# Optimization experiments

Measured on AMD Instinct MI355X. Metric: run time of the kernel, lower is better.

The kernel has to match this reference:

```python
import jax, jax.numpy as jnp
import numpy as np

NU, NI, E = 200000, 100000, 500000
D, H, O = 128, 256, 128  # embedding_dim, hidden_dim, output_dim


def _sage(x_src, x_dst, src, dst, n_dst, W_l, b_l, W_r):
    """PyG SAGEConv (mean aggr): lin_l(mean_j x_src[j]) + lin_r(x_dst)."""
    msgs = x_src[src]                                            # [E, d_in]
    summed = jax.ops.segment_sum(msgs, dst, num_segments=n_dst)  # [n_dst, d_in]
    deg = jax.ops.segment_sum(jnp.ones(src.shape, x_src.dtype), dst, num_segments=n_dst)
    mean = summed / jnp.maximum(deg, 1.0)[:, None]
    return mean @ W_l + b_l + x_dst @ W_r


def setup_inputs() -> dict:
    key = jax.random.key(0)
    ks = jax.random.split(key, 18)

    def w(k, i, o):
        return jax.random.normal(k, (i, o), jnp.float32) / np.float32(np.sqrt(i))

    return {
        "x_user": jax.random.normal(ks[0], (NU, D), jnp.float32),
        "x_item": jax.random.normal(ks[1], (NI, D), jnp.float32),
        "edge_src": jax.random.randint(ks[2], (E,), 0, NU, jnp.int32),
        "edge_dst": jax.random.randint(ks[3], (E,), 0, NI, jnp.int32),
        # layer 1 (encoder): D -> H, one SAGEConv per edge type
        "W_l1_ui": w(ks[4], D, H), "W_r1_ui": w(ks[5], D, H), "b_l1_ui": jnp.zeros((H,), jnp.float32),
        "W_l1_iu": w(ks[6], D, H), "W_r1_iu": w(ks[7], D, H), "b_l1_iu": jnp.zeros((H,), jnp.float32),
        # layer 2 (projection): H -> O
        "W_l2_ui": w(ks[8], H, O), "W_r2_ui": w(ks[9], H, O), "b_l2_ui": jnp.zeros((O,), jnp.float32),
        "W_l2_iu": w(ks[10], H, O), "W_r2_iu": w(ks[11], H, O), "b_l2_iu": jnp.zeros((O,), jnp.float32),
    }


def reference(x_user, x_item, edge_src, edge_dst,
              W_l1_ui, W_r1_ui, b_l1_ui, W_l1_iu, W_r1_iu, b_l1_iu,
              W_l2_ui, W_r2_ui, b_l2_ui, W_l2_iu, W_r2_iu, b_l2_iu):
    # encoder layer: relu(SAGEConv) per destination node type (dropout=eval/no-op)
    h_item = jax.nn.relu(_sage(x_user, x_item, edge_src, edge_dst, NI, W_l1_ui, b_l1_ui, W_r1_ui))
    h_user = jax.nn.relu(_sage(x_item, x_user, edge_dst, edge_src, NU, W_l1_iu, b_l1_iu, W_r1_iu))
    # extra relu in RecommendationGNN.forward is a no-op after relu
    # projection layer: relu(SAGEConv), dropout=0
    o_item = jax.nn.relu(_sage(h_user, h_item, edge_src, edge_dst, NI, W_l2_ui, b_l2_ui, W_r2_ui))
    o_user = jax.nn.relu(_sage(h_item, h_user, edge_dst, edge_src, NU, W_l2_iu, b_l2_iu, W_r2_iu))
    return (o_user, o_item)
```

## Files before the change

kernel.cpp:

```cpp
#include <hip/hip_runtime.h>
#include <stdint.h>

typedef __attribute__((ext_vector_type(8))) short short8;
typedef __attribute__((ext_vector_type(4))) float f32x4;

#define SCAN_TILE 4096

__device__ __forceinline__ float bf2f(unsigned short u) {
  union { unsigned int i; float f; } v;
  v.i = ((unsigned int)u) << 16;
  return v.f;
}
__device__ __forceinline__ unsigned short f2bf(float f) {
  union { float f; unsigned int i; } v;
  v.f = f;
  unsigned int u = v.i;
  return (unsigned short)((u + 0x7FFFu + ((u >> 16) & 1u)) >> 16);
}
__device__ __forceinline__ unsigned int pack2(float a, float b) {
  return (unsigned int)f2bf(a) | ((unsigned int)f2bf(b) << 16);
}
__device__ __forceinline__ void add2(float& a, float& b, unsigned int v) {
  a += bf2f((unsigned short)(v & 0xffff));
  b += bf2f((unsigned short)(v >> 16));
}

__device__ __forceinline__ size_t fragS128(int row, int k) {
  return ((size_t)(row >> 4) * 4 + (size_t)(k >> 5)) * 512
       + (size_t)((((row & 15) + (((k >> 3) & 3) << 4)) << 3) + (k & 7));
}

__global__ __launch_bounds__(256) void build_wt_all(
    const float* __restrict__ Wl1ui, const float* __restrict__ Wr1ui,
    const float* __restrict__ Wl1iu, const float* __restrict__ Wr1iu,
    const float* __restrict__ Wl2ui, const float* __restrict__ Wr2ui,
    const float* __restrict__ Wl2iu, const float* __restrict__ Wr2iu,
    unsigned short* __restrict__ T1ui_l, unsigned short* __restrict__ T1ui_h,
    unsigned short* __restrict__ T1iu_l, unsigned short* __restrict__ T1iu_h,
    unsigned short* __restrict__ T2lui_l, unsigned short* __restrict__ T2lui_h,
    unsigned short* __restrict__ T2rui_l, unsigned short* __restrict__ T2rui_h,
    unsigned short* __restrict__ T2liu_l, unsigned short* __restrict__ T2liu_h,
    unsigned short* __restrict__ T2riu_l, unsigned short* __restrict__ T2riu_h)
{
  int idx = blockIdx.x * 256 + threadIdx.x;
  const float *W1, *W2;
  unsigned short *lo, *hi;
  int N, rel;
  if (idx < 65536)       { W1 = Wl1ui; W2 = Wr1ui;          lo = T1ui_l;  hi = T1ui_h;  N = 256; rel = idx; }
  else if (idx < 131072) { W1 = Wl1iu; W2 = Wr1iu;          lo = T1iu_l;  hi = T1iu_h;  N = 256; rel = idx - 65536; }
  else if (idx < 163840) { W1 = Wl2ui; W2 = Wl2ui + 128*128; lo = T2lui_l; hi = T2lui_h; N = 128; rel = idx - 131072; }
  else if (idx < 196608) { W1 = Wr2ui; W2 = Wr2ui + 128*128; lo = T2rui_l; hi = T2rui_h; N = 128; rel = idx - 163840; }
  else if (idx < 229376) { W1 = Wl2iu; W2 = Wl2iu + 128*128; lo = T2liu_l; hi = T2liu_h; N = 128; rel = idx - 196608; }
  else                   { W1 = Wr2iu; W2 = Wr2iu + 128*128; lo = T2riu_l; hi = T2riu_h; N = 128; rel = idx - 229376; }
  int n = rel >> 8;
  int k = rel & 255;
  float v = (k < 128) ? W1[(size_t)k * N + n] : W2[(size_t)(k - 128) * N + n];
  if (k < 128) lo[fragS128(n, k)] = f2bf(v);
  else         hi[fragS128(n, k - 128)] = f2bf(v);
}

__global__ __launch_bounds__(256) void conv_x(
    const float* __restrict__ xu, const float* __restrict__ xi,
    uint4* __restrict__ XfI, uint4* __restrict__ XfU,
    int NI, int NU, int MI, int MU)
{
  int u = blockIdx.x * 256 + threadIdx.x;
  int unitsI = MI * 16;
  const float* x; uint4* Xf; int M; int rel;
  if (u < unitsI) { x = xi; Xf = XfI; M = NI; rel = u; }
  else {
    rel = u - unitsI;
    if (rel >= MU * 16) return;
    x = xu; Xf = XfU; M = NU;
  }
  int c = rel >> 6;
  int s = rel & 63;
  int row = ((c >> 2) << 4) + (s & 15);
  int k = ((c & 3) << 5) + ((s >> 4) << 3);
  uint4 o = make_uint4(0u, 0u, 0u, 0u);
  if (row < M) {
    f32x4 a = *(const f32x4*)(x + (size_t)row * 128 + k);
    f32x4 b = *(const f32x4*)(x + (size_t)row * 128 + k + 4);
    o.x = pack2(a[0], a[1]); o.y = pack2(a[2], a[3]);
    o.z = pack2(b[0], b[1]); o.w = pack2(b[2], b[3]);
  }
  Xf[rel] = o;
}

__global__ __launch_bounds__(256) void hist(
    const int* __restrict__ esrc, const int* __restrict__ edst,
    int* __restrict__ cntAll, int NI, int E)
{
  int e = blockIdx.x * 256 + threadIdx.x;
  if (e >= E) return;
  atomicAdd(&cntAll[edst[e]], 1);
  atomicAdd(&cntAll[NI + esrc[e]], 1);
}

__global__ __launch_bounds__(256) void scan_p1(
    const int* __restrict__ cnt, int* __restrict__ tileSums, int NA)
{
  __shared__ int red[256];
  int b = blockIdx.x, t = threadIdx.x;
  int base = b * SCAN_TILE;
  int s = 0;
  for (int i = t; i < SCAN_TILE; i += 256) {
    int g = base + i;
    if (g < NA) s += cnt[g];
  }
  red[t] = s;
  __syncthreads();
  for (int d = 128; d > 0; d >>= 1) {
    if (t < d) red[t] += red[t + d];
    __syncthreads();
  }
  if (t == 0) tileSums[b] = red[0];
}

__global__ __launch_bounds__(256) void scan_p2(
    int* __restrict__ tileSums, int nTiles, int* __restrict__ offEnd)
{
  __shared__ int buf[256];
  int t = threadIdx.x;
  int v = (t < nTiles) ? tileSums[t] : 0;
  buf[t] = v;
  __syncthreads();
  for (int d = 1; d < 256; d <<= 1) {
    int x = (t >= d) ? buf[t - d] : 0;
    __syncthreads();
    buf[t] += x;
    __syncthreads();
  }
  if (t < nTiles) tileSums[t] = buf[t] - v;
  if (t == nTiles - 1) *offEnd = buf[t];
}

__global__ __launch_bounds__(256) void scan_p3(
    const int* __restrict__ cnt, const int* __restrict__ tileSums,
    int* __restrict__ off, int NA)
{
  __shared__ int red[256];
  int b = blockIdx.x, t = threadIdx.x;
  int base = b * SCAN_TILE + t * 16;
  int loc[16];
  int s = 0;
#pragma unroll
  for (int i = 0; i < 16; ++i) {
    int g = base + i;
    loc[i] = (g < NA) ? cnt[g] : 0;
    s += loc[i];
  }
  red[t] = s;
  __syncthreads();
  for (int d = 1; d < 256; d <<= 1) {
    int x = (t >= d) ? red[t - d] : 0;
    __syncthreads();
    red[t] += x;
    __syncthreads();
  }
  int run = tileSums[b] + red[t] - s;
#pragma unroll
  for (int i = 0; i < 16; ++i) {
    int g = base + i;
    if (g < NA) off[g] = run;
    run += loc[i];
  }
}

__global__ __launch_bounds__(256) void fill_idx(
    const int* __restrict__ esrc, const int* __restrict__ edst,
    const int* __restrict__ offAll, int* __restrict__ curAll,
    int* __restrict__ idxAll, int NI, int E)
{
  int e = blockIdx.x * 256 + threadIdx.x;
  if (e >= E) return;
  int s = esrc[e], d = edst[e];
  int pI = offAll[d] + atomicAdd(&curAll[d], 1);
  idxAll[pI] = s;
  int pU = offAll[NI + s] + atomicAdd(&curAll[NI + s], 1);
  idxAll[pU] = d;
}

__global__ __launch_bounds__(256) void build_mean(
    const float* __restrict__ xu, const float* __restrict__ xi,
    const int* __restrict__ idxAll, const int* __restrict__ offAll,
    unsigned short* __restrict__ MfI, unsigned short* __restrict__ MfU,
    int NI, int NA)
{
  int w2 = (blockIdx.x * 256 + threadIdx.x) >> 6;
  int l = threadIdx.x & 63;
  int h = l >> 5;
  int lh = l & 31;
  int node = w2 * 2 + h;
  if (node >= NA) return;
  bool isItem = (node < NI);
  const float* xo = isItem ? xu : xi;
  unsigned short* Mf = isItem ? MfI : MfU;
  int n = isItem ? node : (node - NI);
  int s = offAll[node], e = offAll[node + 1];

  f32x4 acc = (f32x4){0.f, 0.f, 0.f, 0.f};
  int j = s;
  for (; j + 1 < e; j += 2) {
    int g0 = idxAll[j];
    int g1 = idxAll[j + 1];
    f32x4 v0 = *(const f32x4*)(xo + (size_t)g0 * 128 + lh * 4);
    f32x4 v1 = *(const f32x4*)(xo + (size_t)g1 * 128 + lh * 4);
    acc += v0 + v1;
  }
  if (j < e) {
    int g = idxAll[j];
    acc += *(const f32x4*)(xo + (size_t)g * 128 + lh * 4);
  }

  float inv = 1.0f / (float)max(e - s, 1);
  uint2 o;
  o.x = pack2(acc[0] * inv, acc[1] * inv);
  o.y = pack2(acc[2] * inv, acc[3] * inv);
  *(uint2*)(Mf + fragS128(n, lh * 4)) = o;
}

__global__ __launch_bounds__(256) void seg_mean(
    const unsigned int* __restrict__ pU, const unsigned int* __restrict__ pI,
    const int* __restrict__ idxAll, const int* __restrict__ offAll,
    unsigned int* __restrict__ m2I, unsigned int* __restrict__ m2U,
    int NI, int NA)
{
  int w4 = (blockIdx.x * 256 + threadIdx.x) >> 6;
  int l = threadIdx.x & 63;
  int q = l >> 4;
  int lq = l & 15;
  int node = w4 * 4 + q;
  if (node >= NA) return;
  bool isItem = (node < NI);
  const unsigned int* p = isItem ? pU : pI;
  unsigned int* m2 = isItem ? m2I : m2U;
  int n = isItem ? node : (node - NI);
  int s = offAll[node], e = offAll[node + 1];

  float a0 = 0.f, a1 = 0.f, a2 = 0.f, a3 = 0.f,
        a4 = 0.f, a5 = 0.f, a6 = 0.f, a7 = 0.f;

  int j = s;
  for (; j + 1 < e; j += 2) {
    int g0 = idxAll[j];
    int g1 = idxAll[j + 1];
    uint4 v0 = *(const uint4*)(p + (size_t)g0 * 64 + lq * 4);
    uint4 v1 = *(const uint4*)(p + (size_t)g1 * 64 + lq * 4);
    add2(a0, a1, v0.x); add2(a2, a3, v0.y); add2(a4, a5, v0.z); add2(a6, a7, v0.w);
    add2(a0, a1, v1.x); add2(a2, a3, v1.y); add2(a4, a5, v1.z); add2(a6, a7, v1.w);
  }
  if (j < e) {
    int g = idxAll[j];
    uint4 v = *(const uint4*)(p + (size_t)g * 64 + lq * 4);
    add2(a0, a1, v.x); add2(a2, a3, v.y); add2(a4, a5, v.z); add2(a6, a7, v.w);
  }

  float inv = 1.0f / (float)max(e - s, 1);
  uint4 o;
  o.x = pack2(a0 * inv, a1 * inv);
  o.y = pack2(a2 * inv, a3 * inv);
  o.z = pack2(a4 * inv, a5 * inv);
  o.w = pack2(a6 * inv, a7 * inv);
  *(uint4*)(m2 + (size_t)n * 64 + lq * 4) = o;
}

struct GemmP {
  const unsigned short* Alo; const unsigned short* Ahi;
  const unsigned short* Blo; const unsigned short* Bhi;
  const float* bias;
  const unsigned short* Madd;
  void* outp; unsigned short* outHi;
  int M;
};

__global__ __launch_bounds__(256) void gemm_flat(
    GemmP P0, GemmP P1, int rb0,
    int outF32, int outFrag, int N, int doRelu)
{
  __shared__ __attribute__((aligned(16))) uint4 lds4[2048];

  const int bx = blockIdx.x;
  const bool first = (bx < rb0);
  GemmP P = first ? P0 : P1;
  const int mb = first ? bx : bx - rb0;

  const int tid = threadIdx.x;
  const int lane = tid & 63;
  const int wave = tid >> 6;
  const int nBase = blockIdx.y * 128;
  const int r16 = lane & 15;
  const int quad = lane >> 4;

  const uint4* AL = (const uint4*)P.Alo;
  const uint4* AH = (const uint4*)P.Ahi;
  const uint4* BL = (const uint4*)P.Blo + (size_t)(nBase >> 4) * 256;
  const uint4* BH = (const uint4*)P.Bhi + (size_t)(nBase >> 4) * 256;

  const int fa = wave * 2;

#define STAGE(s, b) do {                                                        \
    const uint4* As_ = ((s) < 4 ? AL : AH);                                     \
    const uint4* Bs_ = ((s) < 4 ? BL : BH);                                     \
    const int k0_ = (s) & 3;                                                    \
    const uint4* ga0 = As_ + ((size_t)((mb * 8 + fa) * 4 + k0_)) * 64 + lane;   \
    const uint4* ga1 = As_ + ((size_t)((mb * 8 + fa + 1) * 4 + k0_)) * 64 + lane;\
    const uint4* gb0 = Bs_ + ((size_t)(fa * 4 + k0_)) * 64 + lane;              \
    const uint4* gb1 = Bs_ + ((size_t)((fa + 1) * 4 + k0_)) * 64 + lane;        \
    __builtin_amdgcn_global_load_lds(                                           \
        (const __attribute__((address_space(1))) void*)ga0,                     \
        (__attribute__((address_space(3))) void*)&lds4[(b) * 1024 + fa * 64], 16, 0, 0); \
    __builtin_amdgcn_global_load_lds(                                           \
        (const __attribute__((address_space(1))) void*)ga1,                     \
        (__attribute__((address_space(3))) void*)&lds4[(b) * 1024 + (fa + 1) * 64], 16, 0, 0); \
    __builtin_amdgcn_global_load_lds(                                           \
        (const __attribute__((address_space(1))) void*)gb0,                     \
        (__attribute__((address_space(3))) void*)&lds4[(b) * 1024 + 512 + fa * 64], 16, 0, 0); \
    __builtin_amdgcn_global_load_lds(                                           \
        (const __attribute__((address_space(1))) void*)gb1,                     \
        (__attribute__((address_space(3))) void*)&lds4[(b) * 1024 + 512 + (fa + 1) * 64], 16, 0, 0); \
  } while (0)

  f32x4 acc[4][4];
#pragma unroll
  for (int i = 0; i < 4; ++i)
#pragma unroll
    for (int j = 0; j < 4; ++j) acc[i][j] = (f32x4){0.f, 0.f, 0.f, 0.f};

  STAGE(0, 0);
  STAGE(1, 1);

  const int wr = (wave >> 1) * 4;
  const int wc = (wave & 1) * 4;

#pragma unroll
  for (int s = 0; s < 8; ++s) {
    const int b = s & 1;
    if (s < 7) asm volatile("s_waitcnt vmcnt(4)\ns_barrier" ::: "memory");
    else       asm volatile("s_waitcnt vmcnt(0)\ns_barrier" ::: "memory");

    short8 av[4], bv[4];
#pragma unroll
    for (int g = 0; g < 4; ++g) {
      uint4 ta = lds4[b * 1024 + (wr + g) * 64 + lane];
      uint4 tb = lds4[b * 1024 + 512 + (wc + g) * 64 + lane];
      av[g] = *(const short8*)&ta;
      bv[g] = *(const short8*)&tb;
    }
#pragma unroll
    for (int mg = 0; mg < 4; ++mg)
#pragma unroll
      for (int ng = 0; ng < 4; ++ng)
        acc[mg][ng] = __builtin_amdgcn_mfma_f32_16x16x32_bf16(bv[ng], av[mg], acc[mg][ng], 0, 0, 0);

    if (s < 6) {
      asm volatile("s_waitcnt lgkmcnt(0)\ns_barrier" ::: "memory");
      STAGE(s + 2, b);
    }
  }
#undef STAGE

  const int m0 = mb * 128 + (wave >> 1) * 64;
  const int n0 = nBase + (wave & 1) * 64;
#pragma unroll
  for (int mg = 0; mg < 4; ++mg) {
    int row = m0 + mg * 16 + r16;
    if (row < P.M) {
#pragma unroll
      for (int ng = 0; ng < 4; ++ng) {
        int col = n0 + ng * 16 + quad * 4;
        f32x4 v = acc[mg][ng];
        if (P.bias) {
          f32x4 b4 = *(const f32x4*)(P.bias + col);
          v += b4;
        }
        if (P.Madd) {
          uint2 md = *(const uint2*)(P.Madd + (size_t)row * 128 + col);
          v[0] += bf2f((unsigned short)(md.x & 0xffff));
          v[1] += bf2f((unsigned short)(md.x >> 16));
          v[2] += bf2f((unsigned short)(md.y & 0xffff));
          v[3] += bf2f((unsigned short)(md.y >> 16));
        }
        if (doRelu) {
          v[0] = fmaxf(v[0], 0.0f); v[1] = fmaxf(v[1], 0.0f);
          v[2] = fmaxf(v[2], 0.0f); v[3] = fmaxf(v[3], 0.0f);
        }
        if (outF32) {
          *(f32x4*)((float*)P.outp + (size_t)row * N + col) = v;
        } else {
          uint2 o;
          o.x = pack2(v[0], v[1]);
          o.y = pack2(v[2], v[3]);
          if (outFrag) {
            if (col < 128) *(uint2*)((unsigned short*)P.outp + fragS128(row, col)) = o;
            else           *(uint2*)(P.outHi + fragS128(row, col - 128)) = o;
          } else {
            *(uint2*)((unsigned short*)P.outp + (size_t)row * N + col) = o;
          }
        }
      }
    }
  }
}

extern "C" void kernel_launch(void* const* d_in, const int* in_sizes, int n_in,
                              void* d_out, int out_size, void* d_ws, size_t ws_size,
                              hipStream_t stream)
{
  const float* x_user  = (const float*)d_in[0];
  const float* x_item  = (const float*)d_in[1];
  const int*   esrc    = (const int*)d_in[2];
  const int*   edst    = (const int*)d_in[3];
  const float* W_l1_ui = (const float*)d_in[4];
  const float* W_r1_ui = (const float*)d_in[5];
  const float* b_l1_ui = (const float*)d_in[6];
  const float* W_l1_iu = (const float*)d_in[7];
  const float* W_r1_iu = (const float*)d_in[8];
  const float* b_l1_iu = (const float*)d_in[9];
  const float* W_l2_ui = (const float*)d_in[10];
  const float* W_r2_ui = (const float*)d_in[11];
  const float* b_l2_ui = (const float*)d_in[12];
  const float* W_l2_iu = (const float*)d_in[13];
  const float* W_r2_iu = (const float*)d_in[14];
  const float* b_l2_iu = (const float*)d_in[15];

  const int NU = in_sizes[0] / 128;
  const int NI = in_sizes[1] / 128;
  const int E  = in_sizes[2];
  const int NA = NI + NU;
  const int MI = ((NI + 127) / 128) * 128;
  const int MU = ((NU + 127) / 128) * 128;

  char* ws = (char*)d_ws;
  size_t off = 0;
  auto alloc = [&](size_t bytes) -> void* {
    void* p = ws + off;
    off += (bytes + 255) & ~(size_t)255;
    return p;
  };

  int* cntAll = (int*)alloc((size_t)NA * 4);
  int* curAll = (int*)alloc((size_t)NA * 4);
  size_t zeroBytes = off;
  int* offAll   = (int*)alloc((size_t)(NA + 1) * 4);
  int* tileSums = (int*)alloc(256 * 4);
  int* idxAll   = (int*)alloc((size_t)2 * E * 4);
  unsigned short* T1ui_l  = (unsigned short*)alloc(256 * 128 * 2);
  unsigned short* T1ui_h  = (unsigned short*)alloc(256 * 128 * 2);
  unsigned short* T1iu_l  = (unsigned short*)alloc(256 * 128 * 2);
  unsigned short* T1iu_h  = (unsigned short*)alloc(256 * 128 * 2);
  unsigned short* T2lui_l = (unsigned short*)alloc(128 * 128 * 2);
  unsigned short* T2lui_h = (unsigned short*)alloc(128 * 128 * 2);
  unsigned short* T2rui_l = (unsigned short*)alloc(128 * 128 * 2);
  unsigned short* T2rui_h = (unsigned short*)alloc(128 * 128 * 2);
  unsigned short* T2liu_l = (unsigned short*)alloc(128 * 128 * 2);
  unsigned short* T2liu_h = (unsigned short*)alloc(128 * 128 * 2);
  unsigned short* T2riu_l = (unsigned short*)alloc(128 * 128 * 2);
  unsigned short* T2riu_h = (unsigned short*)alloc(128 * 128 * 2);
  unsigned short* h_item = (unsigned short*)alloc((size_t)MI * 256 * 2);
  unsigned short* h_item_hi = h_item + (size_t)MI * 128;
  unsigned short* h_user = (unsigned short*)alloc((size_t)MU * 256 * 2);
  unsigned short* h_user_hi = h_user + (size_t)MU * 128;
  char* R = (char*)alloc((size_t)(MI + MU) * 256 * 2);
  unsigned short* Mf_item = (unsigned short*)R;
  unsigned short* Mf_user = (unsigned short*)(R + (size_t)MI * 128 * 2);
  unsigned short* Xf_item = (unsigned short*)(R + (size_t)(MI + MU) * 128 * 2);
  unsigned short* Xf_user = (unsigned short*)(R + (size_t)(2 * MI + MU) * 128 * 2);
  unsigned short* p_user = (unsigned short*)R;
  unsigned short* p_item = (unsigned short*)(R + (size_t)NU * 128 * 2);
  unsigned short* m2I    = (unsigned short*)(R + (size_t)(NU + NI) * 128 * 2);
  unsigned short* m2U    = (unsigned short*)(R + (size_t)(NU + 2 * NI) * 128 * 2);

  float* out = (float*)d_out;

  hipMemsetAsync(ws, 0, zeroBytes, stream);

  build_wt_all<<<1024, 256, 0, stream>>>(
      W_l1_ui, W_r1_ui, W_l1_iu, W_r1_iu, W_l2_ui, W_r2_ui, W_l2_iu, W_r2_iu,
      T1ui_l, T1ui_h, T1iu_l, T1iu_h,
      T2lui_l, T2lui_h, T2rui_l, T2rui_h, T2liu_l, T2liu_h, T2riu_l, T2riu_h);

  int units = (MI + MU) * 16;
  conv_x<<<(units + 255) / 256, 256, 0, stream>>>(
      x_user, x_item, (uint4*)Xf_item, (uint4*)Xf_user, NI, NU, MI, MU);

  int egrid = (E + 255) / 256;
  int nTiles = (NA + SCAN_TILE - 1) / SCAN_TILE;
  hist<<<egrid, 256, 0, stream>>>(esrc, edst, cntAll, NI, E);
  scan_p1<<<nTiles, 256, 0, stream>>>(cntAll, tileSums, NA);
  scan_p2<<<1, 256, 0, stream>>>(tileSums, nTiles, offAll + NA);
  scan_p3<<<nTiles, 256, 0, stream>>>(cntAll, tileSums, offAll, NA);
  fill_idx<<<egrid, 256, 0, stream>>>(esrc, edst, offAll, curAll, idxAll, NI, E);

  int waves1 = (NA + 1) / 2;
  build_mean<<<(waves1 * 64 + 255) / 256, 256, 0, stream>>>(
      x_user, x_item, idxAll, offAll, Mf_item, Mf_user, NI, NA);

  const int rbI = MI / 128, rbU = MU / 128;

  GemmP l1i = {Mf_item, Xf_item, T1ui_l, T1ui_h, b_l1_ui, nullptr, h_item, h_item_hi, NI};
  GemmP l1u = {Mf_user, Xf_user, T1iu_l, T1iu_h, b_l1_iu, nullptr, h_user, h_user_hi, NU};
  gemm_flat<<<dim3(rbI + rbU, 2), 256, 0, stream>>>(l1i, l1u, rbI, 0, 1, 256, 1);

  GemmP pi = {h_item, h_item_hi, T2liu_l, T2liu_h, nullptr, nullptr, p_item, nullptr, NI};
  GemmP pu = {h_user, h_user_hi, T2lui_l, T2lui_h, nullptr, nullptr, p_user, nullptr, NU};
  gemm_flat<<<dim3(rbI + rbU, 1), 256, 0, stream>>>(pi, pu, rbI, 0, 0, 128, 0);

  int waves2 = (NA + 3) / 4;
  seg_mean<<<(waves2 * 64 + 255) / 256, 256, 0, stream>>>(
      (const unsigned int*)p_user, (const unsigned int*)p_item,
      idxAll, offAll, (unsigned int*)m2I, (unsigned int*)m2U, NI, NA);

  GemmP oi = {h_item, h_item_hi, T2rui_l, T2rui_h, b_l2_ui, m2I,
              out + (size_t)NU * 128, nullptr, NI};
  GemmP ou = {h_user, h_user_hi, T2riu_l, T2riu_h, b_l2_iu, m2U,
              out, nullptr, NU};
  gemm_flat<<<dim3(rbI + rbU, 1), 256, 0, stream>>>(oi, ou, rbI, 1, 0, 128, 1);
}
```

Measured before the change: 828.7 us.

## Make GEMM waves independent with private LDS slices and no block barriers

The GEMM block shrinks from four waves sharing 128x128 tiles to two waves, each computing a 64x64 output tile from its own private LDS double buffer. Because no wave reads data loaded by another wave, the s_barrier instructions are dropped and only per-wave vmcnt/lgkmcnt waits remain. The launch grid doubles along N to cover the same output. The cost is that A and B tiles are no longer shared across waves, so each wave loads its own, raising global/L2 traffic per FLOP.

```diff
diff --git a/kernel.cpp b/kernel.cpp
--- a/kernel.cpp
+++ b/kernel.cpp
@@ -274,7 +274,7 @@
   int M;
 };
 
-__global__ __launch_bounds__(256) void gemm_flat(
+__global__ __launch_bounds__(128) void gemm_flat(
     GemmP P0, GemmP P1, int rb0,
     int outF32, int outFrag, int N, int doRelu)
 {
@@ -288,38 +288,33 @@
   const int tid = threadIdx.x;
   const int lane = tid & 63;
   const int wave = tid >> 6;
-  const int nBase = blockIdx.y * 128;
+  const int nb = blockIdx.y;
   const int r16 = lane & 15;
   const int quad = lane >> 4;
 
   const uint4* AL = (const uint4*)P.Alo;
   const uint4* AH = (const uint4*)P.Ahi;
-  const uint4* BL = (const uint4*)P.Blo + (size_t)(nBase >> 4) * 256;
-  const uint4* BH = (const uint4*)P.Bhi + (size_t)(nBase >> 4) * 256;
-
-  const int fa = wave * 2;
-
-#define STAGE(s, b) do {                                                        \
-    const uint4* As_ = ((s) < 4 ? AL : AH);                                     \
-    const uint4* Bs_ = ((s) < 4 ? BL : BH);                                     \
-    const int k0_ = (s) & 3;                                                    \
-    const uint4* ga0 = As_ + ((size_t)((mb * 8 + fa) * 4 + k0_)) * 64 + lane;   \
-    const uint4* ga1 = As_ + ((size_t)((mb * 8 + fa + 1) * 4 + k0_)) * 64 + lane;\
-    const uint4* gb0 = Bs_ + ((size_t)(fa * 4 + k0_)) * 64 + lane;              \
-    const uint4* gb1 = Bs_ + ((size_t)((fa + 1) * 4 + k0_)) * 64 + lane;        \
-    __builtin_amdgcn_global_load_lds(                                           \
-        (const __attribute__((address_space(1))) void*)ga0,                     \
-        (__attribute__((address_space(3))) void*)&lds4[(b) * 1024 + fa * 64], 16, 0, 0); \
-    __builtin_amdgcn_global_load_lds(                                           \
-        (const __attribute__((address_space(1))) void*)ga1,                     \
-        (__attribute__((address_space(3))) void*)&lds4[(b) * 1024 + (fa + 1) * 64], 16, 0, 0); \
-    __builtin_amdgcn_global_load_lds(                                           \
-        (const __attribute__((address_space(1))) void*)gb0,                     \
-        (__attribute__((address_space(3))) void*)&lds4[(b) * 1024 + 512 + fa * 64], 16, 0, 0); \
-    __builtin_amdgcn_global_load_lds(                                           \
-        (const __attribute__((address_space(1))) void*)gb1,                     \
-        (__attribute__((address_space(3))) void*)&lds4[(b) * 1024 + 512 + (fa + 1) * 64], 16, 0, 0); \
-  } while (0)
+  const uint4* BL = (const uint4*)P.Blo;
+  const uint4* BH = (const uint4*)P.Bhi;
+
+  const int rgb = mb * 8 + wave * 4;
+  const int cgb = nb * 4;
+  const int wbase = wave * 1024;
+
+  auto STAGE = [&](int s, int b) {
+    const uint4* As_ = (s < 4) ? AL : AH;
+    const uint4* Bs_ = (s < 4) ? BL : BH;
+    const int k0_ = s & 3;
+#pragma unroll
+    for (int g = 0; g < 4; ++g) {
+      __builtin_amdgcn_global_load_lds(
+          (const __attribute__((address_space(1))) void*)(As_ + (size_t)((rgb + g) * 4 + k0_) * 64 + lane),
+          (__attribute__((address_space(3))) void*)&lds4[wbase + b * 512 + g * 64], 16, 0, 0);
+      __builtin_amdgcn_global_load_lds(
+          (const __attribute__((address_space(1))) void*)(Bs_ + (size_t)((cgb + g) * 4 + k0_) * 64 + lane),
+          (__attribute__((address_space(3))) void*)&lds4[wbase + b * 512 + 256 + g * 64], 16, 0, 0);
+    }
+  };
 
   f32x4 acc[4][4];
 #pragma unroll
@@ -330,20 +325,17 @@
   STAGE(0, 0);
   STAGE(1, 1);
 
-  const int wr = (wave >> 1) * 4;
-  const int wc = (wave & 1) * 4;
-
 #pragma unroll
   for (int s = 0; s < 8; ++s) {
     const int b = s & 1;
-    if (s < 7) asm volatile("s_waitcnt vmcnt(4)\ns_barrier" ::: "memory");
-    else       asm volatile("s_waitcnt vmcnt(0)\ns_barrier" ::: "memory");
+    if (s < 7) asm volatile("s_waitcnt vmcnt(8)" ::: "memory");
+    else       asm volatile("s_waitcnt vmcnt(0)" ::: "memory");
 
     short8 av[4], bv[4];
 #pragma unroll
     for (int g = 0; g < 4; ++g) {
-      uint4 ta = lds4[b * 1024 + (wr + g) * 64 + lane];
-      uint4 tb = lds4[b * 1024 + 512 + (wc + g) * 64 + lane];
+      uint4 ta = lds4[wbase + b * 512 + g * 64 + lane];
+      uint4 tb = lds4[wbase + b * 512 + 256 + g * 64 + lane];
       av[g] = *(const short8*)&ta;
       bv[g] = *(const short8*)&tb;
     }
@@ -354,14 +346,13 @@
         acc[mg][ng] = __builtin_amdgcn_mfma_f32_16x16x32_bf16(bv[ng], av[mg], acc[mg][ng], 0, 0, 0);
 
     if (s < 6) {
-      asm volatile("s_waitcnt lgkmcnt(0)\ns_barrier" ::: "memory");
+      asm volatile("s_waitcnt lgkmcnt(0)" ::: "memory");
       STAGE(s + 2, b);
     }
   }
-#undef STAGE
-
-  const int m0 = mb * 128 + (wave >> 1) * 64;
-  const int n0 = nBase + (wave & 1) * 64;
+
+  const int m0 = mb * 128 + wave * 64;
+  const int n0 = nb * 64;
 #pragma unroll
   for (int mg = 0; mg < 4; ++mg) {
     int row = m0 + mg * 16 + r16;
@@ -500,11 +491,11 @@
 
   GemmP l1i = {Mf_item, Xf_item, T1ui_l, T1ui_h, b_l1_ui, nullptr, h_item, h_item_hi, NI};
   GemmP l1u = {Mf_user, Xf_user, T1iu_l, T1iu_h, b_l1_iu, nullptr, h_user, h_user_hi, NU};
-  gemm_flat<<<dim3(rbI + rbU, 2), 256, 0, stream>>>(l1i, l1u, rbI, 0, 1, 256, 1);
+  gemm_flat<<<dim3(rbI + rbU, 4), 128, 0, stream>>>(l1i, l1u, rbI, 0, 1, 256, 1);
 
   GemmP pi = {h_item, h_item_hi, T2liu_l, T2liu_h, nullptr, nullptr, p_item, nullptr, NI};
   GemmP pu = {h_user, h_user_hi, T2lui_l, T2lui_h, nullptr, nullptr, p_user, nullptr, NU};
-  gemm_flat<<<dim3(rbI + rbU, 1), 256, 0, stream>>>(pi, pu, rbI, 0, 0, 128, 0);
+  gemm_flat<<<dim3(rbI + rbU, 2), 128, 0, stream>>>(pi, pu, rbI, 0, 0, 128, 0);
 
   int waves2 = (NA + 3) / 4;
   seg_mean<<<(waves2 * 64 + 255) / 256, 256, 0, stream>>>(
@@ -515,5 +506,5 @@
               out + (size_t)NU * 128, nullptr, NI};
   GemmP ou = {h_user, h_user_hi, T2riu_l, T2riu_h, b_l2_iu, m2U,
               out, nullptr, NU};
-  gemm_flat<<<dim3(rbI + rbU, 1), 256, 0, stream>>>(oi, ou, rbI, 1, 0, 128, 1);
-}
+  gemm_flat<<<dim3(rbI + rbU, 2), 128, 0, stream>>>(oi, ou, rbI, 1, 0, 128, 1);
+}
```

Measured after the change: 898.1 us. 1.08x slower.
